# Performance work log

Hardware: AMD Instinct MI355X
Metric: run time of the kernel (lower is better)

## Reference

```python
import jax, jax.numpy as jnp
import numpy as np

D_MODEL = 1024
NUM_HEAD = 16
LN_EPS = 1e-5


def _layernorm(x, w, b):
    mu = jnp.mean(x, axis=-1, keepdims=True)
    var = jnp.mean(jnp.square(x - mu), axis=-1, keepdims=True)
    return (x - mu) * jax.lax.rsqrt(var + LN_EPS) * w + b


def setup_inputs() -> dict:
    key = jax.random.key(0)
    ks = jax.random.split(key, 8)
    d = D_MODEL
    s = 1.0 / np.sqrt(d)
    return {
        "text": jax.random.normal(ks[0], (8, 512, d), dtype=jnp.float32),
        "av_feat": jax.random.normal(ks[1], (8, 1024, d), dtype=jnp.float32),
        "tn_w": jnp.ones((d,), jnp.float32),
        "tn_b": jnp.zeros((d,), jnp.float32),
        "an_w": jnp.ones((d,), jnp.float32),
        "an_b": jnp.zeros((d,), jnp.float32),
        "Wq": jax.random.uniform(ks[2], (d, d), jnp.float32, -s, s),
        "bq": jnp.zeros((d,), jnp.float32),
        "Wk": jax.random.uniform(ks[3], (d, d), jnp.float32, -s, s),
        "bk": jnp.zeros((d,), jnp.float32),
        "Wv": jax.random.uniform(ks[4], (d, d), jnp.float32, -s, s),
        "bv": jnp.zeros((d,), jnp.float32),
    }


def reference(text, av_feat, tn_w, tn_b, an_w, an_b, Wq, bq, Wk, bk, Wv, bv):
    bs, num_word, d_model = text.shape
    num_valid = av_feat.shape[1]
    h = NUM_HEAD
    d_k = d_model // h

    t = _layernorm(text, tn_w, tn_b)
    a = _layernorm(av_feat, an_w, an_b)

    # torch Linear: x @ W.T + b
    q = (t @ Wq.T + bq).reshape(bs, num_word, h, d_k)   # b q h d
    k = (a @ Wk.T + bk).reshape(bs, num_valid, h, d_k)  # b k h d
    v = (a @ Wv.T + bv).reshape(bs, num_valid, h, d_k)  # b k h d

    # sigmoid attention (no softmax): scores (bs, num_word, num_valid, num_head)
    attn = jnp.einsum('bqhd,bkhd->bqkh', q, k) / np.sqrt(d_k)
    attn = jax.nn.sigmoid(attn)

    # out = sum over num_valid of attn * v -> (bs, num_word, num_head, d_k)
    out = jnp.einsum('bqkh,bkhd->bqhd', attn, v).reshape(bs, num_word, d_model)
    return out, attn.mean(-1)
```

## Files before the change

### kernel.cpp

```cpp
#include <hip/hip_runtime.h>
#include <hip/hip_bf16.h>
#include <math.h>

typedef float f32x4 __attribute__((ext_vector_type(4)));
typedef short s16x8 __attribute__((ext_vector_type(8)));
typedef unsigned short us;

typedef const __attribute__((address_space(1))) unsigned int* gas1_t;
typedef __attribute__((address_space(3))) unsigned int* las3_t;

__device__ __forceinline__ void load_lds16(const void* g, void* l) {
  __builtin_amdgcn_global_load_lds((gas1_t)g, (las3_t)l, 16, 0, 0);
}

__device__ __forceinline__ us f2bf(float f) {
  union { float f; unsigned u; } v; v.f = f;
  unsigned u = v.u;
  u += 0x7fffu + ((u >> 16) & 1u);
  return (us)(u >> 16);
}

__global__ __launch_bounds__(256) void prep_kernel(
    const float* __restrict__ text, const float* __restrict__ av,
    const float* __restrict__ tn_w, const float* __restrict__ tn_b,
    const float* __restrict__ an_w, const float* __restrict__ an_b,
    const float* __restrict__ Wq, const float* __restrict__ Wk, const float* __restrict__ Wv,
    us* __restrict__ Tln, us* __restrict__ Aln,
    us* __restrict__ Wqb, us* __restrict__ Wkb, us* __restrict__ Wvb) {
  int id = blockIdx.x, tid = threadIdx.x;
  if (id >= 12288) {
    int c = id - 12288;
    const float* src; us* dst;
    if (c < 1024)      { src = Wq; dst = Wqb; }
    else if (c < 2048) { src = Wk; dst = Wkb; c -= 1024; }
    else               { src = Wv; dst = Wvb; c -= 2048; }
    int i = c * 256 + tid;
    float4 v = ((const float4*)src)[i];
    ushort4 o;
    o.x = f2bf(v.x); o.y = f2bf(v.y); o.z = f2bf(v.z); o.w = f2bf(v.w);
    ((ushort4*)dst)[i] = o;
    return;
  }
  const float *x, *w, *b; us* outp; int row;
  if (id < 4096) { x = text; w = tn_w; b = tn_b; outp = Tln; row = id; }
  else           { x = av;   w = an_w; b = an_b; outp = Aln; row = id - 4096; }
  const float4* xr = (const float4*)(x + (size_t)row * 1024);
  float4 v = xr[tid];
  float s  = v.x + v.y + v.z + v.w;
  float ss = v.x * v.x + v.y * v.y + v.z * v.z + v.w * v.w;
  #pragma unroll
  for (int off = 32; off; off >>= 1) {
    s  += __shfl_down(s, off);
    ss += __shfl_down(ss, off);
  }
  __shared__ float red[8];
  int wid = tid >> 6, lane = tid & 63;
  if (lane == 0) { red[wid] = s; red[wid + 4] = ss; }
  __syncthreads();
  s  = red[0] + red[1] + red[2] + red[3];
  ss = red[4] + red[5] + red[6] + red[7];
  float mu  = s * (1.0f / 1024.0f);
  float var = ss * (1.0f / 1024.0f) - mu * mu;
  float rstd = rsqrtf(var + 1e-5f);
  float4 wv = ((const float4*)w)[tid];
  float4 bv = ((const float4*)b)[tid];
  ushort4 o;
  o.x = f2bf((v.x - mu) * rstd * wv.x + bv.x);
  o.y = f2bf((v.y - mu) * rstd * wv.y + bv.y);
  o.z = f2bf((v.z - mu) * rstd * wv.z + bv.z);
  o.w = f2bf((v.w - mu) * rstd * wv.w + bv.w);
  ((ushort4*)(outp + (size_t)row * 1024))[tid] = o;
}

__global__ __launch_bounds__(256) void gemm3_kernel(
    const us* __restrict__ Tln, const us* __restrict__ Aln,
    const us* __restrict__ Wqb, const us* __restrict__ Wkb, const us* __restrict__ Wvb,
    const float* __restrict__ bq, const float* __restrict__ bk_, const float* __restrict__ bv_,
    us* __restrict__ Qb, us* __restrict__ Kb, us* __restrict__ Vtb) {
  __shared__ us As[2][128 * 32];
  __shared__ us Bs[2][128 * 32];
  const int K = 1024, N = 1024;
  int id = blockIdx.x;
  const us *A, *B; const float* bias; us* C; bool trans = false;
  int rb, cb;
  if (id < 256)      { A = Tln; B = Wqb; bias = bq;  C = Qb;  rb = id >> 3; cb = id & 7; }
  else if (id < 768) { id -= 256; A = Aln; B = Wkb; bias = bk_; C = Kb; rb = id >> 3; cb = id & 7; }
  else               { id -= 768; A = Aln; B = Wvb; bias = bv_; C = Vtb; rb = id >> 3; cb = id & 7; trans = true; }
  int row0 = rb * 128, col0 = cb * 128;
  int tid = threadIdx.x, lane = tid & 63, wid = tid >> 6;
  int wr = wid >> 1, wc = wid & 1;
  int l15 = lane & 15, kof = (lane >> 4) * 8, lg = lane >> 4;
  int ch0 = wid * 64 + lane, ch1 = ch0 + 256;
  int r0 = ch0 >> 2, c0 = ch0 & 3, r1 = ch1 >> 2, c1 = ch1 & 3;

#define G3_STAGE(buf, kt)                                                       \
  { load_lds16(&A[(size_t)(row0 + r0) * K + (kt) + c0 * 8], &As[buf][ch0 * 8]); \
    load_lds16(&B[(size_t)(col0 + r0) * K + (kt) + c0 * 8], &Bs[buf][ch0 * 8]); \
    load_lds16(&A[(size_t)(row0 + r1) * K + (kt) + c1 * 8], &As[buf][ch1 * 8]); \
    load_lds16(&B[(size_t)(col0 + r1) * K + (kt) + c1 * 8], &Bs[buf][ch1 * 8]); }

  f32x4 acc[4][4] = {};
  G3_STAGE(0, 0);
  __syncthreads();
  int cur = 0;
  for (int kt = 0; kt < K; kt += 32) {
    if (kt + 32 < K) G3_STAGE(cur ^ 1, kt + 32);
    s16x8 af[4], bfr[4];
    #pragma unroll
    for (int m = 0; m < 4; ++m)
      af[m] = *(const s16x8*)&As[cur][(wr * 64 + m * 16 + l15) * 32 + kof];
    #pragma unroll
    for (int n = 0; n < 4; ++n)
      bfr[n] = *(const s16x8*)&Bs[cur][(wc * 64 + n * 16 + l15) * 32 + kof];
    #pragma unroll
    for (int m = 0; m < 4; ++m)
      #pragma unroll
      for (int n = 0; n < 4; ++n)
        acc[m][n] = __builtin_amdgcn_mfma_f32_16x16x32_bf16(af[m], bfr[n], acc[m][n], 0, 0, 0);
    __syncthreads();
    cur ^= 1;
  }
  if (trans) {
    int b = row0 >> 10;
    int kbase = (row0 & 1023) + wr * 64 + lg * 4;
    #pragma unroll
    for (int n = 0; n < 4; ++n) {
      int col = col0 + wc * 64 + n * 16 + l15;
      float bb = bias[col];
      us* cp = C + (size_t)b * 1048576 + (size_t)col * 1024 + kbase;
      #pragma unroll
      for (int m = 0; m < 4; ++m) {
        ushort4 o;
        o.x = f2bf(acc[m][n][0] + bb);
        o.y = f2bf(acc[m][n][1] + bb);
        o.z = f2bf(acc[m][n][2] + bb);
        o.w = f2bf(acc[m][n][3] + bb);
        *(ushort4*)(cp + m * 16) = o;
      }
    }
  } else {
    #pragma unroll
    for (int n = 0; n < 4; ++n) {
      int col = col0 + wc * 64 + n * 16 + l15;
      float bb = bias[col];
      #pragma unroll
      for (int m = 0; m < 4; ++m)
        #pragma unroll
        for (int j = 0; j < 4; ++j) {
          int row = row0 + wr * 64 + m * 16 + lg * 4 + j;
          C[(size_t)row * N + col] = f2bf(acc[m][n][j] + bb);
        }
    }
  }
#undef G3_STAGE
}

#define PSTR 40
#define PBUF (16 * 16 * PSTR)
__global__ __launch_bounds__(1024, 4) void attn_kernel(
    const us* __restrict__ Q, const us* __restrict__ K,
    const us* __restrict__ Vt, float* __restrict__ out,
    float* __restrict__ meanout) {
  __shared__ us Plds[2 * PBUF];
  int bid = blockIdx.x;
  int b = bid & 7, qt = bid >> 3;
  int q0 = qt * 16;
  int tid = threadIdx.x, lane = tid & 63, h = tid >> 6;
  int l15 = lane & 15, lg = lane >> 4;

  const us* Qp = Q + (size_t)(b * 512 + q0) * 1024 + h * 64;
  const us* Kp = K + (size_t)b * 1048576 + h * 64;
  const us* Vp = Vt + (size_t)b * 1048576 + (size_t)(h * 64) * 1024;

  s16x8 aq0 = *(const s16x8*)(Qp + (size_t)l15 * 1024 + lg * 8);
  s16x8 aq1 = *(const s16x8*)(Qp + (size_t)l15 * 1024 + 32 + lg * 8);

  f32x4 oacc[4] = {};
  const float SC = -0.1803368801111244f;
  const us* Kl = Kp + (size_t)l15 * 1024 + lg * 8;
  const us* Vl = Vp + (size_t)l15 * 1024 + lg * 8;

  s16x8 bkA[2][2], bkB[2][2];
  #pragma unroll
  for (int kc = 0; kc < 2; ++kc)
    #pragma unroll
    for (int ks = 0; ks < 2; ++ks)
      bkA[kc][ks] = *(const s16x8*)(Kl + (size_t)(kc * 16) * 1024 + ks * 32);

#define ATTN_STEP(KT, BKU, BKP, BUF)                                              \
  {                                                                               \
                            \
    s16x8 bvv[4];                                                                 \
    _Pragma("unroll")                                                             \
    for (int nd = 0; nd < 4; ++nd)                                                \
      bvv[nd] = *(const s16x8*)(Vl + (size_t)(nd * 16) * 1024 + (KT));            \
                                                                   \
    f32x4 s0 = {}, s1 = {};                                                       \
    s0 = __builtin_amdgcn_mfma_f32_16x16x32_bf16(aq0, BKU[0][0], s0, 0, 0, 0);    \
    s0 = __builtin_amdgcn_mfma_f32_16x16x32_bf16(aq1, BKU[0][1], s0, 0, 0, 0);    \
    s1 = __builtin_amdgcn_mfma_f32_16x16x32_bf16(aq0, BKU[1][0], s1, 0, 0, 0);    \
    s1 = __builtin_amdgcn_mfma_f32_16x16x32_bf16(aq1, BKU[1][1], s1, 0, 0, 0);    \
                                                \
    if ((KT) + 32 < 1024) {                                                       \
      _Pragma("unroll")                                                           \
      for (int kc = 0; kc < 2; ++kc)                                              \
        _Pragma("unroll")                                                         \
        for (int ks = 0; ks < 2; ++ks)                                            \
          BKP[kc][ks] = *(const s16x8*)(Kl + (size_t)((KT) + 32 + kc * 16) * 1024 + ks * 32); \
    }                                                                             \
                                              \
    us* Ph = Plds + (BUF) * PBUF + h * (16 * PSTR);                               \
    _Pragma("unroll")                                                             \
    for (int j = 0; j < 4; ++j) {                                                 \
      float p0 = __builtin_amdgcn_rcpf(1.0f + exp2f(s0[j] * SC));                 \
      float p1 = __builtin_amdgcn_rcpf(1.0f + exp2f(s1[j] * SC));                 \
      Ph[(lg * 4 + j) * PSTR + l15]      = f2bf(p0);                              \
      Ph[(lg * 4 + j) * PSTR + 16 + l15] = f2bf(p1);                              \
    }                                                                             \
    __syncthreads();                                                              \
                    \
    if (tid < 256) {                                                              \
      int q = tid >> 4, pr = tid & 15;                                            \
      const us* pp = Plds + (BUF) * PBUF + q * PSTR + pr * 2;                     \
      float m0 = 0.f, m1 = 0.f;                                                   \
      _Pragma("unroll")                                                           \
      for (int hh = 0; hh < 16; ++hh) {                                           \
        unsigned u = *(const unsigned*)(pp + hh * (16 * PSTR));                   \
        union { unsigned u; float f; } lo, hi;                                    \
        lo.u = u << 16; hi.u = u & 0xffff0000u;                                   \
        m0 += lo.f; m1 += hi.f;                                                   \
      }                                                                           \
      float2 mo; mo.x = m0 * 0.0625f; mo.y = m1 * 0.0625f;                        \
      *(float2*)&meanout[(size_t)(b * 512 + q0 + q) * 1024 + (KT) + pr * 2] = mo; \
    }                                                                             \
                                                                    \
    s16x8 pa = *(const s16x8*)(Ph + l15 * PSTR + lg * 8);                         \
    _Pragma("unroll")                                                             \
    for (int nd = 0; nd < 4; ++nd)                                                \
      oacc[nd] = __builtin_amdgcn_mfma_f32_16x16x32_bf16(pa, bvv[nd], oacc[nd], 0, 0, 0); \
  }

  for (int kt = 0; kt < 1024; kt += 64) {
    ATTN_STEP(kt,      bkA, bkB, 0);
    ATTN_STEP(kt + 32, bkB, bkA, 1);
  }
#undef ATTN_STEP

  #pragma unroll
  for (int nd = 0; nd < 4; ++nd)
    #pragma unroll
    for (int j = 0; j < 4; ++j) {
      int q = lg * 4 + j, d = h * 64 + nd * 16 + l15;
      out[(size_t)(b * 512 + q0 + q) * 1024 + d] = oacc[nd][j];
    }
}

extern "C" void kernel_launch(void* const* d_in, const int* in_sizes, int n_in,
                              void* d_out, int out_size, void* d_ws, size_t ws_size,
                              hipStream_t stream) {
  const float* text = (const float*)d_in[0];
  const float* av   = (const float*)d_in[1];
  const float* tn_w = (const float*)d_in[2];
  const float* tn_b = (const float*)d_in[3];
  const float* an_w = (const float*)d_in[4];
  const float* an_b = (const float*)d_in[5];
  const float* Wq   = (const float*)d_in[6];
  const float* bq   = (const float*)d_in[7];
  const float* Wk   = (const float*)d_in[8];
  const float* bk   = (const float*)d_in[9];
  const float* Wv   = (const float*)d_in[10];
  const float* bv   = (const float*)d_in[11];

  char* ws = (char*)d_ws;
  const size_t MB = 1u << 20;
  us* Wqb = (us*)(ws + 0 * MB);
  us* Wkb = (us*)(ws + 2 * MB);
  us* Wvb = (us*)(ws + 4 * MB);
  us* Tln = (us*)(ws + 6 * MB);
  us* Aln = (us*)(ws + 14 * MB);
  us* Qb  = (us*)(ws + 30 * MB);
  us* Kb  = (us*)(ws + 38 * MB);
  us* Vtb = (us*)(ws + 54 * MB);

  float* out  = (float*)d_out;
  float* mout = out + (size_t)8 * 512 * 1024;

  prep_kernel<<<15360, 256, 0, stream>>>(text, av, tn_w, tn_b, an_w, an_b,
                                         Wq, Wk, Wv, Tln, Aln, Wqb, Wkb, Wvb);
  gemm3_kernel<<<1280, 256, 0, stream>>>(Tln, Aln, Wqb, Wkb, Wvb,
                                         bq, bk, bv, Qb, Kb, Vtb);
  attn_kernel<<<256, 1024, 0, stream>>>(Qb, Kb, Vtb, out, mout);
}
```

Measured before the change: 323.1 us.

## Restructure sigmoid attention into per-wave multi-head, split-key register pipeline

The attention kernel is reorganised so each wave handles four heads over half of the key range. The score MFMA is transposed so the sigmoid probabilities land directly in the B-operand register layout, removing the per-step LDS round trip for P. Head means are partly reduced in registers before a smaller LDS exchange, and the two key halves are merged through an LDS output buffer at the end. The QKV GEMM block indices are also remapped to change which row and column tiles run together, aiming for better cache locality. The cost is fewer waves per CU, higher register pressure and an extra reduction phase.

```diff
diff --git a/kernel.cpp b/kernel.cpp
--- a/kernel.cpp
+++ b/kernel.cpp
@@ -83,9 +83,19 @@
   int id = blockIdx.x;
   const us *A, *B; const float* bias; us* C; bool trans = false;
   int rb, cb;
-  if (id < 256)      { A = Tln; B = Wqb; bias = bq;  C = Qb;  rb = id >> 3; cb = id & 7; }
-  else if (id < 768) { id -= 256; A = Aln; B = Wkb; bias = bk_; C = Kb; rb = id >> 3; cb = id & 7; }
-  else               { id -= 768; A = Aln; B = Wvb; bias = bv_; C = Vtb; rb = id >> 3; cb = id & 7; trans = true; }
+  if (id < 256) {
+    A = Tln; B = Wqb; bias = bq; C = Qb;
+    int x = id & 7, y = id >> 3;
+    rb = x * 4 + (y >> 3); cb = y & 7;
+  } else if (id < 768) {
+    int l = id - 256; A = Aln; B = Wkb; bias = bk_; C = Kb;
+    int x = l & 7, y = l >> 3;
+    rb = x * 8 + (y >> 3); cb = y & 7;
+  } else {
+    int l = id - 768; A = Aln; B = Wvb; bias = bv_; C = Vtb; trans = true;
+    int x = l & 7, y = l >> 3;
+    rb = x * 8 + (y >> 3); cb = y & 7;
+  }
   int row0 = rb * 128, col0 = cb * 128;
   int tid = threadIdx.x, lane = tid & 63, wid = tid >> 6;
   int wr = wid >> 1, wc = wid & 1;
@@ -155,104 +165,139 @@
 #undef G3_STAGE
 }
 
-#define PSTR 40
-#define PBUF (16 * 16 * PSTR)
-__global__ __launch_bounds__(1024, 4) void attn_kernel(
+#define MSTR 34
+__global__ __launch_bounds__(512, 2) void attn_kernel(
     const us* __restrict__ Q, const us* __restrict__ K,
     const us* __restrict__ Vt, float* __restrict__ out,
     float* __restrict__ meanout) {
-  __shared__ us Plds[2 * PBUF];
+  __shared__ float Obuf[16 * 513];
+  __shared__ us Mbuf[2][2][4][16 * MSTR];
   int bid = blockIdx.x;
   int b = bid & 7, qt = bid >> 3;
   int q0 = qt * 16;
-  int tid = threadIdx.x, lane = tid & 63, h = tid >> 6;
+  int tid = threadIdx.x, lane = tid & 63, wv = tid >> 6;
+  int g = wv >> 1, s = wv & 1;
   int l15 = lane & 15, lg = lane >> 4;
-
-  const us* Qp = Q + (size_t)(b * 512 + q0) * 1024 + h * 64;
-  const us* Kp = K + (size_t)b * 1048576 + h * 64;
-  const us* Vp = Vt + (size_t)b * 1048576 + (size_t)(h * 64) * 1024;
-
-  s16x8 aq0 = *(const s16x8*)(Qp + (size_t)l15 * 1024 + lg * 8);
-  s16x8 aq1 = *(const s16x8*)(Qp + (size_t)l15 * 1024 + 32 + lg * 8);
-
-  f32x4 oacc[4] = {};
   const float SC = -0.1803368801111244f;
-  const us* Kl = Kp + (size_t)l15 * 1024 + lg * 8;
-  const us* Vl = Vp + (size_t)l15 * 1024 + lg * 8;
-
-  s16x8 bkA[2][2], bkB[2][2];
+
+  s16x8 aq[4][2];
   #pragma unroll
-  for (int kc = 0; kc < 2; ++kc)
+  for (int hh = 0; hh < 4; ++hh)
     #pragma unroll
     for (int ks = 0; ks < 2; ++ks)
-      bkA[kc][ks] = *(const s16x8*)(Kl + (size_t)(kc * 16) * 1024 + ks * 32);
-
-#define ATTN_STEP(KT, BKU, BKP, BUF)                                              \
-  {                                                                               \
-                            \
-    s16x8 bvv[4];                                                                 \
-    _Pragma("unroll")                                                             \
-    for (int nd = 0; nd < 4; ++nd)                                                \
-      bvv[nd] = *(const s16x8*)(Vl + (size_t)(nd * 16) * 1024 + (KT));            \
-                                                                   \
-    f32x4 s0 = {}, s1 = {};                                                       \
-    s0 = __builtin_amdgcn_mfma_f32_16x16x32_bf16(aq0, BKU[0][0], s0, 0, 0, 0);    \
-    s0 = __builtin_amdgcn_mfma_f32_16x16x32_bf16(aq1, BKU[0][1], s0, 0, 0, 0);    \
-    s1 = __builtin_amdgcn_mfma_f32_16x16x32_bf16(aq0, BKU[1][0], s1, 0, 0, 0);    \
-    s1 = __builtin_amdgcn_mfma_f32_16x16x32_bf16(aq1, BKU[1][1], s1, 0, 0, 0);    \
-                                                \
-    if ((KT) + 32 < 1024) {                                                       \
-      _Pragma("unroll")                                                           \
-      for (int kc = 0; kc < 2; ++kc)                                              \
-        _Pragma("unroll")                                                         \
-        for (int ks = 0; ks < 2; ++ks)                                            \
-          BKP[kc][ks] = *(const s16x8*)(Kl + (size_t)((KT) + 32 + kc * 16) * 1024 + ks * 32); \
-    }                                                                             \
-                                              \
-    us* Ph = Plds + (BUF) * PBUF + h * (16 * PSTR);                               \
-    _Pragma("unroll")                                                             \
-    for (int j = 0; j < 4; ++j) {                                                 \
-      float p0 = __builtin_amdgcn_rcpf(1.0f + exp2f(s0[j] * SC));                 \
-      float p1 = __builtin_amdgcn_rcpf(1.0f + exp2f(s1[j] * SC));                 \
-      Ph[(lg * 4 + j) * PSTR + l15]      = f2bf(p0);                              \
-      Ph[(lg * 4 + j) * PSTR + 16 + l15] = f2bf(p1);                              \
-    }                                                                             \
-    __syncthreads();                                                              \
-                    \
-    if (tid < 256) {                                                              \
-      int q = tid >> 4, pr = tid & 15;                                            \
-      const us* pp = Plds + (BUF) * PBUF + q * PSTR + pr * 2;                     \
-      float m0 = 0.f, m1 = 0.f;                                                   \
-      _Pragma("unroll")                                                           \
-      for (int hh = 0; hh < 16; ++hh) {                                           \
-        unsigned u = *(const unsigned*)(pp + hh * (16 * PSTR));                   \
-        union { unsigned u; float f; } lo, hi;                                    \
-        lo.u = u << 16; hi.u = u & 0xffff0000u;                                   \
-        m0 += lo.f; m1 += hi.f;                                                   \
-      }                                                                           \
-      float2 mo; mo.x = m0 * 0.0625f; mo.y = m1 * 0.0625f;                        \
-      *(float2*)&meanout[(size_t)(b * 512 + q0 + q) * 1024 + (KT) + pr * 2] = mo; \
-    }                                                                             \
-                                                                    \
-    s16x8 pa = *(const s16x8*)(Ph + l15 * PSTR + lg * 8);                         \
-    _Pragma("unroll")                                                             \
-    for (int nd = 0; nd < 4; ++nd)                                                \
-      oacc[nd] = __builtin_amdgcn_mfma_f32_16x16x32_bf16(pa, bvv[nd], oacc[nd], 0, 0, 0); \
-  }
-
-  for (int kt = 0; kt < 1024; kt += 64) {
-    ATTN_STEP(kt,      bkA, bkB, 0);
-    ATTN_STEP(kt + 32, bkB, bkA, 1);
-  }
-#undef ATTN_STEP
+      aq[hh][ks] = *(const s16x8*)(Q + (size_t)(b * 512 + q0 + l15) * 1024 +
+                                   (g * 4 + hh) * 64 + ks * 32 + lg * 8);
+
+  f32x4 oacc[4][4] = {};
+
+  int klo = 8 * (l15 >> 2) + (l15 & 3);
+  const us* Kbase = K + ((size_t)b * 1024 + s * 512) * 1024;
+  const us* Vbase = Vt + (size_t)b * 1048576 + s * 512;
+
+  for (int t = 0; t < 16; ++t) {
+    int kt = t * 32;
+    s16x8 kf[4][2][2];
+    #pragma unroll
+    for (int hh = 0; hh < 4; ++hh)
+      #pragma unroll
+      for (int hf = 0; hf < 2; ++hf)
+        #pragma unroll
+        for (int ks = 0; ks < 2; ++ks)
+          kf[hh][hf][ks] = *(const s16x8*)(Kbase + (size_t)(kt + klo + hf * 4) * 1024 +
+                                           (g * 4 + hh) * 64 + ks * 32 + lg * 8);
+    f32x4 slo[4], shi[4];
+    #pragma unroll
+    for (int hh = 0; hh < 4; ++hh) {
+      f32x4 z = {};
+      z = __builtin_amdgcn_mfma_f32_16x16x32_bf16(kf[hh][0][0], aq[hh][0], z, 0, 0, 0);
+      slo[hh] = __builtin_amdgcn_mfma_f32_16x16x32_bf16(kf[hh][0][1], aq[hh][1], z, 0, 0, 0);
+      f32x4 z2 = {};
+      z2 = __builtin_amdgcn_mfma_f32_16x16x32_bf16(kf[hh][1][0], aq[hh][0], z2, 0, 0, 0);
+      shi[hh] = __builtin_amdgcn_mfma_f32_16x16x32_bf16(kf[hh][1][1], aq[hh][1], z2, 0, 0, 0);
+    }
+    s16x8 vf[4][4];
+    #pragma unroll
+    for (int hh = 0; hh < 4; ++hh)
+      #pragma unroll
+      for (int nd = 0; nd < 4; ++nd)
+        vf[hh][nd] = *(const s16x8*)(Vbase + (size_t)((g * 4 + hh) * 64 + nd * 16 + l15) * 1024 +
+                                     kt + lg * 8);
+    float p4[8] = {0, 0, 0, 0, 0, 0, 0, 0};
+    s16x8 pb[4];
+    #pragma unroll
+    for (int hh = 0; hh < 4; ++hh) {
+      float pl[4], ph[4];
+      #pragma unroll
+      for (int j = 0; j < 4; ++j) {
+        pl[j] = __builtin_amdgcn_rcpf(1.0f + exp2f(slo[hh][j] * SC));
+        ph[j] = __builtin_amdgcn_rcpf(1.0f + exp2f(shi[hh][j] * SC));
+        p4[j] += pl[j];
+        p4[4 + j] += ph[j];
+      }
+      union { s16x8 v; unsigned u[4]; } pk;
+      asm("v_cvt_pk_bf16_f32 %0, %1, %2" : "=v"(pk.u[0]) : "v"(pl[0]), "v"(pl[1]));
+      asm("v_cvt_pk_bf16_f32 %0, %1, %2" : "=v"(pk.u[1]) : "v"(pl[2]), "v"(pl[3]));
+      asm("v_cvt_pk_bf16_f32 %0, %1, %2" : "=v"(pk.u[2]) : "v"(ph[0]), "v"(ph[1]));
+      asm("v_cvt_pk_bf16_f32 %0, %1, %2" : "=v"(pk.u[3]) : "v"(ph[2]), "v"(ph[3]));
+      pb[hh] = pk.v;
+    }
+    #pragma unroll
+    for (int hh = 0; hh < 4; ++hh)
+      #pragma unroll
+      for (int nd = 0; nd < 4; ++nd)
+        oacc[hh][nd] = __builtin_amdgcn_mfma_f32_16x16x32_bf16(vf[hh][nd], pb[hh], oacc[hh][nd], 0, 0, 0);
+    {
+      us* mb = &Mbuf[t & 1][s][g][l15 * MSTR + 8 * lg];
+      #pragma unroll
+      for (int i = 0; i < 8; ++i) mb[i] = f2bf(p4[i]);
+    }
+    __syncthreads();
+    {
+      int s2 = tid >> 8, q = (tid >> 4) & 15, k2 = (tid & 15) * 2;
+      float m0 = 0.f, m1 = 0.f;
+      #pragma unroll
+      for (int gg = 0; gg < 4; ++gg) {
+        unsigned u = *(const unsigned*)&Mbuf[t & 1][s2][gg][q * MSTR + k2];
+        union { unsigned u; float f; } lo, hi;
+        lo.u = u << 16; hi.u = u & 0xffff0000u;
+        m0 += lo.f; m1 += hi.f;
+      }
+      float2 mo; mo.x = m0 * 0.0625f; mo.y = m1 * 0.0625f;
+      *(float2*)&meanout[(size_t)(b * 512 + q0 + q) * 1024 + s2 * 512 + kt + k2] = mo;
+    }
+  }
 
   #pragma unroll
-  for (int nd = 0; nd < 4; ++nd)
-    #pragma unroll
-    for (int j = 0; j < 4; ++j) {
-      int q = lg * 4 + j, d = h * 64 + nd * 16 + l15;
-      out[(size_t)(b * 512 + q0 + q) * 1024 + d] = oacc[nd][j];
-    }
+  for (int c = 0; c < 2; ++c) {
+    __syncthreads();
+    if ((g >> 1) == c && s == 0) {
+      #pragma unroll
+      for (int hh = 0; hh < 4; ++hh)
+        #pragma unroll
+        for (int nd = 0; nd < 4; ++nd)
+          #pragma unroll
+          for (int j = 0; j < 4; ++j)
+            Obuf[l15 * 513 + ((g & 1) * 4 + hh) * 64 + nd * 16 + lg * 4 + j] = oacc[hh][nd][j];
+    }
+    __syncthreads();
+    if ((g >> 1) == c && s == 1) {
+      #pragma unroll
+      for (int hh = 0; hh < 4; ++hh)
+        #pragma unroll
+        for (int nd = 0; nd < 4; ++nd)
+          #pragma unroll
+          for (int j = 0; j < 4; ++j)
+            Obuf[l15 * 513 + ((g & 1) * 4 + hh) * 64 + nd * 16 + lg * 4 + j] += oacc[hh][nd][j];
+    }
+    __syncthreads();
+    #pragma unroll
+    for (int r = 0; r < 4; ++r) {
+      int flat = tid + r * 512;
+      int q = flat >> 7, c4 = flat & 127;
+      float4 v = *(const float4*)&Obuf[q * 513 + c4 * 4];
+      *(float4*)&out[(size_t)(b * 512 + q0 + q) * 1024 + c * 512 + c4 * 4] = v;
+    }
+  }
 }
 
 extern "C" void kernel_launch(void* const* d_in, const int* in_sizes, int n_in,
@@ -289,5 +334,5 @@
                                          Wq, Wk, Wv, Tln, Aln, Wqb, Wkb, Wvb);
   gemm3_kernel<<<1280, 256, 0, stream>>>(Tln, Aln, Wqb, Wkb, Wvb,
                                          bq, bk, bv, Qb, Kb, Vtb);
-  attn_kernel<<<256, 1024, 0, stream>>>(Qb, Kb, Vtb, out, mout);
-}
+  attn_kernel<<<256, 512, 0, stream>>>(Qb, Kb, Vtb, out, mout);
+}
```

After: 325.2 us. No clear change (+0.6%).
